# Kernel optimization log

Hardware: AMD Instinct MI355X
Metric: run time of the kernel (lower is better)

## Reference

```python
import jax, jax.numpy as jnp
import numpy as np
import math

HIDDEN = 1024
HEADS = 16
HEAD_DIM = HIDDEN // HEADS
RANK = 16
LORA_SCALING = 1.0 / RANK  # loralib default lora_alpha=1 -> scaling = alpha/r


def setup_inputs() -> dict:
    key = jax.random.key(0)
    ks = jax.random.split(key, 16)
    bs, seq = 4, 2048
    inp = {
        "hidden_states": jax.random.normal(ks[0], (bs, seq, HIDDEN), dtype=jnp.float32),
        "attention_mask": jnp.zeros((bs, 1, 1, seq), dtype=jnp.float32),
    }
    s = 0.02
    for i, nm in enumerate(["q", "k", "v"]):
        inp[f"W{nm}"] = jax.random.normal(ks[1 + 4 * i], (HIDDEN, HIDDEN), dtype=jnp.float32) * s
        inp[f"b{nm}"] = jnp.zeros((HIDDEN,), dtype=jnp.float32)
        inp[f"A{nm}"] = jax.random.normal(ks[2 + 4 * i], (RANK, HIDDEN), dtype=jnp.float32) * s
        inp[f"B{nm}"] = jnp.zeros((HIDDEN, RANK), dtype=jnp.float32)  # loralib inits B to zero
    return inp


def _lora_linear(x, W, b, A, B):
    # y = x W^T + b + scaling * (x A^T) B^T
    return x @ W.T + b + LORA_SCALING * ((x @ A.T) @ B.T)


def _transform(x, W, b, A, B, bs, seq):
    proj = _lora_linear(x, W, b, A, B)  # [bs, seq, hidden]
    return proj.reshape(bs, seq, HEADS, HEAD_DIM).transpose(0, 2, 1, 3)  # [bs, h, seq, d]


def reference(hidden_states, attention_mask, Wq, bq, Aq, Bq, Wk, bk, Ak, Bk, Wv, bv, Av, Bv):
    bs, seq, _ = hidden_states.shape
    q = _transform(hidden_states, Wq, bq, Aq, Bq, bs, seq)
    k = _transform(hidden_states, Wk, bk, Ak, Bk, bs, seq)
    v = _transform(hidden_states, Wv, bv, Av, Bv, bs, seq)
    scores = jnp.einsum("bhqd,bhkd->bhqk", q, k) / math.sqrt(HEAD_DIM) + attention_mask
    probs = jax.nn.softmax(scores, axis=-1)  # [bs, h, seq, seq]
    out = jnp.einsum("bhqk,bhkd->bhqd", probs, v)  # [bs, h, seq, d]
    return out.transpose(0, 2, 1, 3).reshape(bs, seq, HIDDEN)
```

## Files before the change

### kernel.cpp

```cpp
#include <hip/hip_runtime.h>
#include <stdint.h>

typedef __bf16 bf16x8 __attribute__((ext_vector_type(8)));
typedef float f32x4 __attribute__((ext_vector_type(4)));
typedef float f32x16 __attribute__((ext_vector_type(16)));

static __device__ __forceinline__ unsigned int pk_bf16(float a, float b) {
  unsigned int d;
  asm("v_cvt_pk_bf16_f32 %0, %1, %2" : "=v"(d) : "v"(a), "v"(b));
  return d;
}
static __device__ __forceinline__ float exp2_hw(float x) {
  float r;
  asm("v_exp_f32 %0, %1" : "=v"(r) : "v"(x));
  return r;
}
static __device__ __forceinline__ float rcp_hw(float x) {
  float r;
  asm("v_rcp_f32 %0, %1" : "=v"(r) : "v"(x));
  return r;
}
static __device__ __forceinline__ void gll16(const void* g, void* l) {
  __builtin_amdgcn_global_load_lds((const __attribute__((address_space(1))) unsigned int*)g,
                                   (__attribute__((address_space(3))) unsigned int*)l,
                                   16, 0, 0);
}

__global__ __launch_bounds__(256) void prep_kernel(
    const float* __restrict__ X, unsigned short* __restrict__ Xbf,
    const float* __restrict__ Wq, const float* __restrict__ Aq, const float* __restrict__ Bq,
    const float* __restrict__ Wk, const float* __restrict__ Ak, const float* __restrict__ Bk,
    const float* __restrict__ Wv, const float* __restrict__ Av, const float* __restrict__ Bv,
    unsigned short* __restrict__ Weff) {
  int bid = blockIdx.x;
  if (bid < 8192) {
    int i = (bid * 256 + threadIdx.x) * 4;
    float4 v = *(const float4*)(X + i);
    uint2 o;
    o.x = pk_bf16(v.x, v.y);
    o.y = pk_bf16(v.z, v.w);
    *(uint2*)(Xbf + i) = o;
  } else {
    int idx = ((bid - 8192) * 256 + threadIdx.x) * 4;
    int p = idx >> 20;
    int o = (idx >> 10) & 1023;
    int i = idx & 1023;
    const float* W = (p == 0) ? Wq : (p == 1) ? Wk : Wv;
    const float* A = (p == 0) ? Aq : (p == 1) ? Ak : Av;
    const float* B = (p == 0) ? Bq : (p == 1) ? Bk : Bv;
    float4 acc = {0.f, 0.f, 0.f, 0.f};
#pragma unroll
    for (int r = 0; r < 16; ++r) {
      float bb = B[o * 16 + r];
      float4 av = *(const float4*)&A[r * 1024 + i];
      acc.x += bb * av.x; acc.y += bb * av.y;
      acc.z += bb * av.z; acc.w += bb * av.w;
    }
    float4 wv = *(const float4*)&W[o * 1024 + i];
    uint2 ov;
    ov.x = pk_bf16(wv.x + acc.x * 0.0625f, wv.y + acc.y * 0.0625f);
    ov.y = pk_bf16(wv.z + acc.z * 0.0625f, wv.w + acc.w * 0.0625f);
    *(uint2*)&Weff[idx] = ov;
  }
}

#define GEMM_BAR()                                   \
  asm volatile("s_waitcnt lgkmcnt(0)" ::: "memory"); \
  __builtin_amdgcn_sched_barrier(0);                 \
  __builtin_amdgcn_s_barrier();                      \
  __builtin_amdgcn_sched_barrier(0);

__global__ __launch_bounds__(256) void gemm_qkv(
    const unsigned short* __restrict__ X, const unsigned short* __restrict__ Weff,
    const float* __restrict__ bq, const float* __restrict__ bk, const float* __restrict__ bv,
    unsigned short* __restrict__ qbuf, unsigned short* __restrict__ kbuf,
    unsigned short* __restrict__ vtbuf) {
  __shared__ __align__(16) unsigned short As[2][128][32];
  __shared__ __align__(16) unsigned short Bs[2][128][32];
  const int K = 1024;
  int tid = threadIdx.x;
  int lane = tid & 63;
  int w = tid >> 6;
  int wm = (w >> 1) * 64;
  int wn = (w & 1) * 64;
  int c = lane & 15;
  int quad = lane >> 4;

  int bid = blockIdx.x;
  int grp = bid / 192;
  int rem = bid % 192;
  int m0 = (grp * 8 + (rem & 7)) * 128;
  int n0 = (rem >> 3) * 128;
  int p = n0 >> 10;

  int ldr = lane >> 2;
  int ldc = (lane & 3) * 8;
  const unsigned short* gA = X + (m0 + w * 32 + ldr) * K + ldc;
  const unsigned short* gB = Weff + (n0 + w * 32 + ldr) * K + ldc;

  f32x4 acc[4][4] = {};

  gll16(gA, &As[0][w * 32][0]);
  gll16(gA + 16 * K, &As[0][w * 32 + 16][0]);
  gll16(gB, &Bs[0][w * 32][0]);
  gll16(gB + 16 * K, &Bs[0][w * 32 + 16][0]);

  if (p == 2) {
    for (int t = 0; t < 32; t++) {
      int cb = t & 1, nb = cb ^ 1;
      if (t < 31) {
        int ko = (t + 1) * 32;
        gll16(gA + ko, &As[nb][w * 32][0]);
        gll16(gA + ko + 16 * K, &As[nb][w * 32 + 16][0]);
        gll16(gB + ko, &Bs[nb][w * 32][0]);
        gll16(gB + ko + 16 * K, &Bs[nb][w * 32 + 16][0]);
        asm volatile("s_waitcnt vmcnt(4)" ::: "memory");
      } else {
        asm volatile("s_waitcnt vmcnt(0)" ::: "memory");
      }
      __builtin_amdgcn_sched_barrier(0);
      __builtin_amdgcn_s_barrier();
      __builtin_amdgcn_sched_barrier(0);
      bf16x8 af[4], bfr[4];
#pragma unroll
      for (int mi = 0; mi < 4; mi++)
        af[mi] = *(const bf16x8*)&As[cb][wm + mi * 16 + c][quad * 8];
#pragma unroll
      for (int ni = 0; ni < 4; ni++)
        bfr[ni] = *(const bf16x8*)&Bs[cb][wn + ni * 16 + c][quad * 8];
#pragma unroll
      for (int mi = 0; mi < 4; mi++)
#pragma unroll
        for (int ni = 0; ni < 4; ni++)
          acc[mi][ni] = __builtin_amdgcn_mfma_f32_16x16x32_bf16(af[mi], bfr[ni], acc[mi][ni], 0, 0, 0);
      GEMM_BAR()
    }
    const float* bias = bv;
#pragma unroll
    for (int ni = 0; ni < 4; ni++) {
      int o = (n0 + wn + ni * 16 + c) & 1023;
      int h = o >> 6;
      int d = o & 63;
      float bval = bias[o];
#pragma unroll
      for (int mi = 0; mi < 4; mi++) {
        int mbase = m0 + wm + mi * 16 + quad * 4;
        int bb = mbase >> 11;
        int s = mbase & 2047;
        uint2 o4;
        o4.x = pk_bf16(acc[mi][ni][0] + bval, acc[mi][ni][1] + bval);
        o4.y = pk_bf16(acc[mi][ni][2] + bval, acc[mi][ni][3] + bval);
        *(uint2*)&vtbuf[((bb * 16 + h) * 64 + d) * 2048 + s] = o4;
      }
    }
  } else {
    for (int t = 0; t < 32; t++) {
      int cb = t & 1, nb = cb ^ 1;
      if (t < 31) {
        int ko = (t + 1) * 32;
        gll16(gA + ko, &As[nb][w * 32][0]);
        gll16(gA + ko + 16 * K, &As[nb][w * 32 + 16][0]);
        gll16(gB + ko, &Bs[nb][w * 32][0]);
        gll16(gB + ko + 16 * K, &Bs[nb][w * 32 + 16][0]);
        asm volatile("s_waitcnt vmcnt(4)" ::: "memory");
      } else {
        asm volatile("s_waitcnt vmcnt(0)" ::: "memory");
      }
      __builtin_amdgcn_sched_barrier(0);
      __builtin_amdgcn_s_barrier();
      __builtin_amdgcn_sched_barrier(0);
      bf16x8 af[4], bfr[4];
#pragma unroll
      for (int mi = 0; mi < 4; mi++)
        af[mi] = *(const bf16x8*)&As[cb][wm + mi * 16 + c][quad * 8];
#pragma unroll
      for (int ni = 0; ni < 4; ni++)
        bfr[ni] = *(const bf16x8*)&Bs[cb][wn + ni * 16 + c][quad * 8];
#pragma unroll
      for (int mi = 0; mi < 4; mi++)
#pragma unroll
        for (int ni = 0; ni < 4; ni++)
          acc[mi][ni] = __builtin_amdgcn_mfma_f32_16x16x32_bf16(bfr[ni], af[mi], acc[mi][ni], 0, 0, 0);
      GEMM_BAR()
    }
    const float* bias = (p == 1) ? bk : bq;
    unsigned short* dst = (p == 1) ? kbuf : qbuf;
#pragma unroll
    for (int mi = 0; mi < 4; mi++) {
      int m = m0 + wm + mi * 16 + c;
      int bb = m >> 11;
      int ss = m & 2047;
#pragma unroll
      for (int ni = 0; ni < 4; ni++) {
        int o = (n0 + wn + ni * 16 + quad * 4) & 1023;
        int h = o >> 6;
        int d = o & 63;
        float4 b4 = *(const float4*)&bias[o];
        uint2 o4;
        o4.x = pk_bf16(acc[mi][ni][0] + b4.x, acc[mi][ni][1] + b4.y);
        o4.y = pk_bf16(acc[mi][ni][2] + b4.z, acc[mi][ni][3] + b4.w);
        *(uint2*)&dst[((bb * 16 + h) * 2048 + ss) * 64 + d] = o4;
      }
    }
  }
}

__global__ __launch_bounds__(512, 4) void attn_kernel(
    const unsigned short* __restrict__ qbuf, const unsigned short* __restrict__ kbuf,
    const unsigned short* __restrict__ vtbuf, const float* __restrict__ maskg,
    float* __restrict__ out) {
  __shared__ __align__(16) unsigned short Ks[2][64][72];
  __shared__ __align__(16) unsigned short Vts[2][64][72];
  __shared__ __align__(16) float masks2[2048];
  __shared__ __align__(16) float lrow[256];

  const float SC = 0.125f * 1.4426950408889634f;
  const float L2E = 1.4426950408889634f;

  int tid = threadIdx.x;
  int lane = tid & 63;
  int w = tid >> 6;
  int m31 = lane & 31;
  int hi = lane >> 5;

  int g = blockIdx.x;
  int qt = (g >> 3) & 7;
  int bh = ((g >> 6) << 3) | (g & 7);
  int b = bh >> 4;
  int h = bh & 15;
  int q0 = qt * 256;

  const unsigned short* Qbh = qbuf + bh * (2048 * 64);
  const unsigned short* Kbh = kbuf + bh * (2048 * 64);
  const unsigned short* Vbh = vtbuf + bh * (64 * 2048);

  {
    int idx = tid * 4;
    float4 mm = *(const float4*)(maskg + b * 2048 + idx);
    float4 mo;
    mo.x = (mm.x - 8.f) * L2E;
    mo.y = (mm.y - 8.f) * L2E;
    mo.z = (mm.z - 8.f) * L2E;
    mo.w = (mm.w - 8.f) * L2E;
    *(float4*)&masks2[idx] = mo;
  }

  bf16x8 qfr[4];
#pragma unroll
  for (int ks = 0; ks < 4; ks++)
    qfr[ks] = *(const bf16x8*)(Qbh + (q0 + w * 32 + m31) * 64 + ks * 16 + hi * 8);

  int r2 = tid >> 3;
  int ch = (tid & 7) * 8;

  {
    uint4 t0 = *(const uint4*)(Kbh + r2 * 64 + ch);
    uint4 t2 = *(const uint4*)(Vbh + r2 * 2048 + ch);
    *(uint4*)&Ks[0][r2][ch] = t0;
    *(uint4*)&Vts[0][r2][ch] = t2;
  }
  uint4 pkv0 = *(const uint4*)(Kbh + (64 + r2) * 64 + ch);
  uint4 pkv2 = *(const uint4*)(Vbh + r2 * 2048 + 64 + ch);

  __syncthreads();

  float lsum = 0.f;
  f32x16 acc_o[2] = {};

  for (int t = 0; t < 32; t++) {
    int cur = t & 1;
    int kt = t * 64;

#pragma unroll
    for (int kb = 0; kb < 2; kb++) {
      f32x16 accs = {};
      __builtin_amdgcn_s_setprio(1);
#pragma unroll
      for (int ks = 0; ks < 4; ks++) {
        bf16x8 kf = *(const bf16x8*)&Ks[cur][kb * 32 + m31][ks * 16 + hi * 8];
        accs = __builtin_amdgcn_mfma_f32_32x32x16_bf16(kf, qfr[ks], accs, 0, 0, 0);
      }
      __builtin_amdgcn_s_setprio(0);

      unsigned int up[4][2];
#pragma unroll
      for (int gg = 0; gg < 4; gg++) {
        float4 m4 = *(const float4*)&masks2[kt + kb * 32 + gg * 8 + hi * 4];
        float p0 = exp2_hw(fmaf(accs[gg * 4 + 0], SC, m4.x));
        float p1 = exp2_hw(fmaf(accs[gg * 4 + 1], SC, m4.y));
        float p2 = exp2_hw(fmaf(accs[gg * 4 + 2], SC, m4.z));
        float p3 = exp2_hw(fmaf(accs[gg * 4 + 3], SC, m4.w));
        lsum += (p0 + p1) + (p2 + p3);
        up[gg][0] = pk_bf16(p0, p1);
        up[gg][1] = pk_bf16(p2, p3);
      }

#pragma unroll
      for (int gp = 0; gp < 2; gp++) {
        union { uint4 u; bf16x8 bv8; } pf;
        unsigned int a0 = up[gp * 2][0], b0 = up[gp * 2 + 1][0];
        unsigned int a1 = up[gp * 2][1], b1 = up[gp * 2 + 1][1];
        asm("v_permlane32_swap_b32 %0, %1" : "+v"(a0), "+v"(b0));
        asm("v_permlane32_swap_b32 %0, %1" : "+v"(a1), "+v"(b1));
        pf.u.x = a0;
        pf.u.y = a1;
        pf.u.z = b0;
        pf.u.w = b1;
        __builtin_amdgcn_s_setprio(1);
#pragma unroll
        for (int db = 0; db < 2; db++) {
          bf16x8 vf = *(const bf16x8*)&Vts[cur][db * 32 + m31][kb * 32 + gp * 16 + hi * 8];
          acc_o[db] = __builtin_amdgcn_mfma_f32_32x32x16_bf16(pf.bv8, vf, acc_o[db], 0, 0, 0);
        }
        __builtin_amdgcn_s_setprio(0);
      }
    }

    if (t < 31) {
      int nb = cur ^ 1;
      *(uint4*)&Ks[nb][r2][ch] = pkv0;
      *(uint4*)&Vts[nb][r2][ch] = pkv2;
    }
    asm volatile("s_waitcnt lgkmcnt(0)" ::: "memory");
    __builtin_amdgcn_sched_barrier(0);
    __builtin_amdgcn_s_barrier();
    __builtin_amdgcn_sched_barrier(0);
    if (t < 31) {
      int kn = (kt + 128) & 2047;
      pkv0 = *(const uint4*)(Kbh + (kn + r2) * 64 + ch);
      pkv2 = *(const uint4*)(Vbh + r2 * 2048 + kn + ch);
    }
  }

  lsum += __shfl_xor(lsum, 32);
  lrow[w * 32 + m31] = lsum;
  __asm__ volatile("" ::: "memory");

#pragma unroll
  for (int gg = 0; gg < 4; gg++) {
    float4 l4 = *(const float4*)&lrow[w * 32 + gg * 8 + hi * 4];
    float i0 = rcp_hw(l4.x), i1 = rcp_hw(l4.y), i2 = rcp_hw(l4.z), i3 = rcp_hw(l4.w);
    int qq = q0 + w * 32 + gg * 8 + hi * 4;
#pragma unroll
    for (int db = 0; db < 2; db++) {
      float* obase = out + (b * 2048 + qq) * 1024 + h * 64 + db * 32 + m31;
      obase[0 * 1024] = acc_o[db][gg * 4 + 0] * i0;
      obase[1 * 1024] = acc_o[db][gg * 4 + 1] * i1;
      obase[2 * 1024] = acc_o[db][gg * 4 + 2] * i2;
      obase[3 * 1024] = acc_o[db][gg * 4 + 3] * i3;
    }
  }
}

extern "C" void kernel_launch(void* const* d_in, const int* in_sizes, int n_in,
                              void* d_out, int out_size, void* d_ws, size_t ws_size,
                              hipStream_t stream) {
  const float* X    = (const float*)d_in[0];
  const float* mask = (const float*)d_in[1];
  const float* Wq = (const float*)d_in[2];
  const float* bq = (const float*)d_in[3];
  const float* Aq = (const float*)d_in[4];
  const float* Bq = (const float*)d_in[5];
  const float* Wk = (const float*)d_in[6];
  const float* bk = (const float*)d_in[7];
  const float* Ak = (const float*)d_in[8];
  const float* Bk = (const float*)d_in[9];
  const float* Wv = (const float*)d_in[10];
  const float* bv = (const float*)d_in[11];
  const float* Av = (const float*)d_in[12];
  const float* Bv = (const float*)d_in[13];

  unsigned short* ws    = (unsigned short*)d_ws;
  unsigned short* Xbf   = ws;
  unsigned short* Weff  = Xbf + 8388608;
  unsigned short* qbuf  = Weff + 3145728;
  unsigned short* kbuf  = qbuf + 8388608;
  unsigned short* vtbuf = kbuf + 8388608;

  prep_kernel<<<dim3(11264), dim3(256), 0, stream>>>(X, Xbf, Wq, Aq, Bq, Wk, Ak, Bk, Wv, Av, Bv, Weff);
  gemm_qkv<<<dim3(1536), dim3(256), 0, stream>>>(Xbf, Weff, bq, bk, bv, qbuf, kbuf, vtbuf);
  attn_kernel<<<dim3(512), dim3(512), 0, stream>>>(qbuf, kbuf, vtbuf, mask, (float*)d_out);
}
```

Before: 270.5 us.

## Deepen QKV GEMM LDS pipeline to four stages with one barrier per step

Moves the QKV projection GEMM from double buffering to a 4-slot LDS ring with three tiles prefetched ahead. Each k-step now uses a single barrier, and the wait for the next tile is placed after the MFMA work. The goal is to hide global-to-LDS latency better and remove one barrier per iteration. The cost is twice the LDS per block (64KB), which may reduce occupancy. Correctness depends on the ring-slot reuse ordering being right.

```diff
diff --git a/kernel.cpp b/kernel.cpp
--- a/kernel.cpp
+++ b/kernel.cpp
@@ -64,19 +64,13 @@
   }
 }
 
-#define GEMM_BAR()                                   \
-  asm volatile("s_waitcnt lgkmcnt(0)" ::: "memory"); \
-  __builtin_amdgcn_sched_barrier(0);                 \
-  __builtin_amdgcn_s_barrier();                      \
-  __builtin_amdgcn_sched_barrier(0);
-
 __global__ __launch_bounds__(256) void gemm_qkv(
     const unsigned short* __restrict__ X, const unsigned short* __restrict__ Weff,
     const float* __restrict__ bq, const float* __restrict__ bk, const float* __restrict__ bv,
     unsigned short* __restrict__ qbuf, unsigned short* __restrict__ kbuf,
     unsigned short* __restrict__ vtbuf) {
-  __shared__ __align__(16) unsigned short As[2][128][32];
-  __shared__ __align__(16) unsigned short Bs[2][128][32];
+  __shared__ __align__(16) unsigned short As[4][128][32];
+  __shared__ __align__(16) unsigned short Bs[4][128][32];
   const int K = 1024;
   int tid = threadIdx.x;
   int lane = tid & 63;
@@ -100,40 +94,49 @@
 
   f32x4 acc[4][4] = {};
 
-  gll16(gA, &As[0][w * 32][0]);
-  gll16(gA + 16 * K, &As[0][w * 32 + 16][0]);
-  gll16(gB, &Bs[0][w * 32][0]);
-  gll16(gB + 16 * K, &Bs[0][w * 32 + 16][0]);
+#pragma unroll
+  for (int pt = 0; pt < 3; pt++) {
+    int ko = pt * 32;
+    gll16(gA + ko, &As[pt][w * 32][0]);
+    gll16(gA + ko + 16 * K, &As[pt][w * 32 + 16][0]);
+    gll16(gB + ko, &Bs[pt][w * 32][0]);
+    gll16(gB + ko + 16 * K, &Bs[pt][w * 32 + 16][0]);
+  }
+  asm volatile("s_waitcnt vmcnt(8)" ::: "memory");
+  __builtin_amdgcn_sched_barrier(0);
+  __builtin_amdgcn_s_barrier();
+  __builtin_amdgcn_sched_barrier(0);
 
   if (p == 2) {
     for (int t = 0; t < 32; t++) {
-      int cb = t & 1, nb = cb ^ 1;
-      if (t < 31) {
-        int ko = (t + 1) * 32;
-        gll16(gA + ko, &As[nb][w * 32][0]);
-        gll16(gA + ko + 16 * K, &As[nb][w * 32 + 16][0]);
-        gll16(gB + ko, &Bs[nb][w * 32][0]);
-        gll16(gB + ko + 16 * K, &Bs[nb][w * 32 + 16][0]);
-        asm volatile("s_waitcnt vmcnt(4)" ::: "memory");
-      } else {
-        asm volatile("s_waitcnt vmcnt(0)" ::: "memory");
-      }
+      int cb = t & 3;
+      if (t < 29) {
+        int ko = (t + 3) * 32;
+        int sb = (t + 3) & 3;
+        gll16(gA + ko, &As[sb][w * 32][0]);
+        gll16(gA + ko + 16 * K, &As[sb][w * 32 + 16][0]);
+        gll16(gB + ko, &Bs[sb][w * 32][0]);
+        gll16(gB + ko + 16 * K, &Bs[sb][w * 32 + 16][0]);
+      }
+      bf16x8 af[4], bfr[4];
+#pragma unroll
+      for (int mi = 0; mi < 4; mi++)
+        af[mi] = *(const bf16x8*)&As[cb][wm + mi * 16 + c][quad * 8];
+#pragma unroll
+      for (int ni = 0; ni < 4; ni++)
+        bfr[ni] = *(const bf16x8*)&Bs[cb][wn + ni * 16 + c][quad * 8];
+#pragma unroll
+      for (int mi = 0; mi < 4; mi++)
+#pragma unroll
+        for (int ni = 0; ni < 4; ni++)
+          acc[mi][ni] = __builtin_amdgcn_mfma_f32_16x16x32_bf16(af[mi], bfr[ni], acc[mi][ni], 0, 0, 0);
+      if (t < 29)       asm volatile("s_waitcnt vmcnt(8)" ::: "memory");
+      else if (t == 29) asm volatile("s_waitcnt vmcnt(4)" ::: "memory");
+      else if (t == 30) asm volatile("s_waitcnt vmcnt(0)" ::: "memory");
+      asm volatile("s_waitcnt lgkmcnt(0)" ::: "memory");
       __builtin_amdgcn_sched_barrier(0);
       __builtin_amdgcn_s_barrier();
       __builtin_amdgcn_sched_barrier(0);
-      bf16x8 af[4], bfr[4];
-#pragma unroll
-      for (int mi = 0; mi < 4; mi++)
-        af[mi] = *(const bf16x8*)&As[cb][wm + mi * 16 + c][quad * 8];
-#pragma unroll
-      for (int ni = 0; ni < 4; ni++)
-        bfr[ni] = *(const bf16x8*)&Bs[cb][wn + ni * 16 + c][quad * 8];
-#pragma unroll
-      for (int mi = 0; mi < 4; mi++)
-#pragma unroll
-        for (int ni = 0; ni < 4; ni++)
-          acc[mi][ni] = __builtin_amdgcn_mfma_f32_16x16x32_bf16(af[mi], bfr[ni], acc[mi][ni], 0, 0, 0);
-      GEMM_BAR()
     }
     const float* bias = bv;
 #pragma unroll
@@ -155,33 +158,34 @@
     }
   } else {
     for (int t = 0; t < 32; t++) {
-      int cb = t & 1, nb = cb ^ 1;
-      if (t < 31) {
-        int ko = (t + 1) * 32;
-        gll16(gA + ko, &As[nb][w * 32][0]);
-        gll16(gA + ko + 16 * K, &As[nb][w * 32 + 16][0]);
-        gll16(gB + ko, &Bs[nb][w * 32][0]);
-        gll16(gB + ko + 16 * K, &Bs[nb][w * 32 + 16][0]);
-        asm volatile("s_waitcnt vmcnt(4)" ::: "memory");
-      } else {
-        asm volatile("s_waitcnt vmcnt(0)" ::: "memory");
-      }
+      int cb = t & 3;
+      if (t < 29) {
+        int ko = (t + 3) * 32;
+        int sb = (t + 3) & 3;
+        gll16(gA + ko, &As[sb][w * 32][0]);
+        gll16(gA + ko + 16 * K, &As[sb][w * 32 + 16][0]);
+        gll16(gB + ko, &Bs[sb][w * 32][0]);
+        gll16(gB + ko + 16 * K, &Bs[sb][w * 32 + 16][0]);
+      }
+      bf16x8 af[4], bfr[4];
+#pragma unroll
+      for (int mi = 0; mi < 4; mi++)
+        af[mi] = *(const bf16x8*)&As[cb][wm + mi * 16 + c][quad * 8];
+#pragma unroll
+      for (int ni = 0; ni < 4; ni++)
+        bfr[ni] = *(const bf16x8*)&Bs[cb][wn + ni * 16 + c][quad * 8];
+#pragma unroll
+      for (int mi = 0; mi < 4; mi++)
+#pragma unroll
+        for (int ni = 0; ni < 4; ni++)
+          acc[mi][ni] = __builtin_amdgcn_mfma_f32_16x16x32_bf16(bfr[ni], af[mi], acc[mi][ni], 0, 0, 0);
+      if (t < 29)       asm volatile("s_waitcnt vmcnt(8)" ::: "memory");
+      else if (t == 29) asm volatile("s_waitcnt vmcnt(4)" ::: "memory");
+      else if (t == 30) asm volatile("s_waitcnt vmcnt(0)" ::: "memory");
+      asm volatile("s_waitcnt lgkmcnt(0)" ::: "memory");
       __builtin_amdgcn_sched_barrier(0);
       __builtin_amdgcn_s_barrier();
       __builtin_amdgcn_sched_barrier(0);
-      bf16x8 af[4], bfr[4];
-#pragma unroll
-      for (int mi = 0; mi < 4; mi++)
-        af[mi] = *(const bf16x8*)&As[cb][wm + mi * 16 + c][quad * 8];
-#pragma unroll
-      for (int ni = 0; ni < 4; ni++)
-        bfr[ni] = *(const bf16x8*)&Bs[cb][wn + ni * 16 + c][quad * 8];
-#pragma unroll
-      for (int mi = 0; mi < 4; mi++)
-#pragma unroll
-        for (int ni = 0; ni < 4; ni++)
-          acc[mi][ni] = __builtin_amdgcn_mfma_f32_16x16x32_bf16(bfr[ni], af[mi], acc[mi][ni], 0, 0, 0);
-      GEMM_BAR()
     }
     const float* bias = (p == 1) ? bk : bq;
     unsigned short* dst = (p == 1) ? kbuf : qbuf;
```

Measured after the change: 284.1 us. +5.0%, slower.
